# Kernel optimization log

Measured on AMD Instinct MI355X. Metric: run time of the kernel, lower is better.

The kernel has to match this reference:

```python
import jax, jax.numpy as jnp
import numpy as np

T, B, D, H = 32, 128, 256, 768
MAX_PONDER = 8
EPS = 0.01


def setup_inputs() -> dict:
    key = jax.random.key(0)
    ks = jax.random.split(key, 6)
    s = 1.0 / np.sqrt(H)
    return {
        "input_": jax.random.normal(ks[0], (T, B, D), jnp.float32),
        "W_ih": jax.random.uniform(ks[1], (H, D + 1), jnp.float32, -s, s),
        "W_hh": jax.random.uniform(ks[2], (H, H), jnp.float32, -s, s),
        "b_ih": jax.random.uniform(ks[3], (H,), jnp.float32, -s, s),
        "b_hh": jax.random.uniform(ks[4], (H,), jnp.float32, -s, s),
        "w_p": jax.random.uniform(ks[5], (H,), jnp.float32, -s, s),
        "b_p": jnp.ones((1,), jnp.float32),  # torch reset_parameters fills ponder bias with 1
    }


def reference(input_, W_ih, W_hh, b_ih, b_hh, w_p, b_p):
    T_, B_, D_ = input_.shape
    H_ = W_hh.shape[0]
    dt = input_.dtype
    hx0 = jnp.zeros((B_, H_), dt)

    def time_step(carry, x_t):
        hx, pcost = carry

        def ponder(c, _):
            hx_i, ah, ahx, sc, spc, mask, flag = c
            # input row with ponder flag (0 on first act step, 1 afterwards)
            x_in = jnp.concatenate([x_t, jnp.full((B_, 1), flag, dt)], axis=1)
            # ponder cost assigned for active rows before update
            spc = jnp.where(mask, -ah, spc)
            hx_new = jnp.tanh(x_in @ W_ih.T + b_ih + hx_i @ W_hh.T + b_hh)
            hx_i = jnp.where(mask[:, None], hx_new, hx_i)
            mf = mask.astype(dt)
            ahx = ahx + mf[:, None] * hx_new  # accum_hx += hx (as in source)
            h = jax.nn.sigmoid(hx_new @ w_p + b_p[0])
            ah2 = ah + mf * h
            p = h - jnp.maximum(ah2 - 1.0, 0.0)
            ahx = ahx + (mf * p)[:, None] * hx_new  # accum_hx += p*hx
            sc = sc + mf
            mask2 = ah2 < (1.0 - EPS)
            return (hx_i, ah2, ahx, sc, spc, mask2, jnp.ones((), dt)), None

        init = (hx,
                jnp.zeros((B_,), dt),           # accum_h
                jnp.zeros((B_, H_), dt),        # accum_hx
                jnp.zeros((B_,), dt),           # step_count
                jnp.zeros((B_,), dt),           # step_ponder_cost
                jnp.ones((B_,), bool),          # selector
                jnp.zeros((), dt))              # flag
        (hx_i, ah, ahx, sc, spc, mask, flag), _ = jax.lax.scan(
            ponder, init, None, length=MAX_PONDER)
        hx_out = ahx / sc[:, None]
        return (hx_out, pcost + spc), (hx_out, sc)

    (hx_last, pcost), (all_hx, steps) = jax.lax.scan(
        time_step, (hx0, jnp.zeros((B_,), dt)), input_)
    # all_hx: [T,B,H], hx: [1,B,H], ponder_cost: [B], ponder_times: [T,B]
    return all_hx, hx_last[None], pcost, steps
```

## Files before the change

### kernel.cpp

```cpp
#include <hip/hip_runtime.h>
#include <math.h>

#define TT 32
#define BB 128
#define DD 256
#define HH 768
#define MAXP 8

#define RG   8
#define RPG  16
#define CB   12
#define CS   64
#define NTH  256
#define NCH  24

#define OFF_LAST  ((size_t)TT * BB * HH)
#define OFF_PCOST (OFF_LAST + (size_t)BB * HH)
#define OFF_STEPS (OFF_PCOST + BB)

#define ASCOPE __HIP_MEMORY_SCOPE_AGENT

typedef __attribute__((ext_vector_type(8))) short s16x8;
typedef __attribute__((ext_vector_type(4))) float f32x4;
typedef unsigned long long ull;

static __device__ __forceinline__ unsigned short f2bf(float f) {
    unsigned u = __float_as_uint(f);
    u = (u + 0x7fffu + ((u >> 16) & 1u)) >> 16;
    return (unsigned short)u;
}
static __device__ __forceinline__ float bf2f(unsigned short h) {
    return __uint_as_float(((unsigned)h) << 16);
}

__launch_bounds__(NTH, 1)
__global__ void act_kernel(const float* __restrict__ x,
                           const float* __restrict__ Wih,
                           const float* __restrict__ Whh,
                           const float* __restrict__ bih,
                           const float* __restrict__ bhh,
                           const float* __restrict__ wpv,
                           const float* __restrict__ bp,
                           float* __restrict__ out,
                           unsigned* __restrict__ flags,
                           ull* __restrict__ hxe,
                           float* __restrict__ zpt)
{
    const int tid  = threadIdx.x;
    const int rg   = blockIdx.x & 7;
    const int cbk  = blockIdx.x >> 3;
    const int r0   = rg * RPG;
    const int c0   = cbk * CS;
    const int CT   = tid >> 6;
    const int lane = tid & 63;
    const int am   = lane & 15;
    const int aq   = lane >> 4;

    __shared__ s16x8 A_s[NCH * 64];
    __shared__ s16x8 WB_s[4 * 8 * 64];
    __shared__ s16x8 xA_s[8 * 64];
    __shared__ unsigned short hxn_s[RPG][72];
    __shared__ float zp4_s[RPG][4];
    __shared__ float zred_s[RPG][13];
    __shared__ float ah_s[RPG], spc_s[RPG], pc_s[RPG], w1p_s[RPG], sc_s[RPG], inv_s[RPG];
    __shared__ int   act_s[RPG];
    __shared__ int   nact_s;
    __shared__ float bias_s[CS], wflag_s[CS], wp_s[CS];
    __shared__ float bp_s;

    s16x8 Breg[NCH];
    {
        const float* wr = Whh + (size_t)(c0 + CT*16 + am) * HH + aq*8;
        for (int ch = 0; ch < NCH; ++ch) {
            float4 a0 = *(const float4*)(wr + ch*32);
            float4 a1 = *(const float4*)(wr + ch*32 + 4);
            union { s16x8 v; unsigned short e[8]; } u;
            u.e[0]=f2bf(a0.x); u.e[1]=f2bf(a0.y); u.e[2]=f2bf(a0.z); u.e[3]=f2bf(a0.w);
            u.e[4]=f2bf(a1.x); u.e[5]=f2bf(a1.y); u.e[6]=f2bf(a1.z); u.e[7]=f2bf(a1.w);
            Breg[ch] = u.v;
        }
    }
    for (int ch = 0; ch < 8; ++ch) {
        const float* wr = Wih + (size_t)(c0 + CT*16 + am) * (DD+1) + ch*32 + aq*8;
        union { s16x8 v; unsigned short e[8]; } u;
        #pragma unroll
        for (int j = 0; j < 8; ++j) u.e[j] = f2bf(wr[j]);
        WB_s[(CT*8 + ch)*64 + lane] = u.v;
    }
    if (tid < CS) {
        bias_s[tid]  = bih[c0+tid] + bhh[c0+tid];
        wflag_s[tid] = Wih[(size_t)(c0+tid)*(DD+1) + DD];
        wp_s[tid]    = wpv[c0+tid];
    }
    if (tid == 0) bp_s = bp[0];
    if (tid < RPG) pc_s[tid] = 0.f;
    {
        s16x8 z8 = {0,0,0,0,0,0,0,0};
        #pragma unroll
        for (int j = 0; j < 6; ++j) A_s[j*NTH + tid] = z8;
    }
    __syncthreads();

    float ahx[48];
    unsigned it = 0;

    for (int t = 0; t < TT; ++t) {
        #pragma unroll
        for (int j = 0; j < 2; ++j) {
            const int s = j*NTH + tid;
            const int ch = s >> 6;
            const float* xb = x + ((size_t)t*BB + r0 + am)*DD + ch*32 + aq*8;
            float4 a0 = *(const float4*)xb;
            float4 a1 = *(const float4*)(xb + 4);
            union { s16x8 v; unsigned short e[8]; } u;
            u.e[0]=f2bf(a0.x); u.e[1]=f2bf(a0.y); u.e[2]=f2bf(a0.z); u.e[3]=f2bf(a0.w);
            u.e[4]=f2bf(a1.x); u.e[5]=f2bf(a1.y); u.e[6]=f2bf(a1.z); u.e[7]=f2bf(a1.w);
            xA_s[s] = u.v;
        }
        if (tid < RPG) { ah_s[tid]=0.f; spc_s[tid]=0.f; sc_s[tid]=0.f; act_s[tid]=1; }
        #pragma unroll
        for (int qq = 0; qq < 48; ++qq) ahx[qq] = 0.f;
        __syncthreads();

        f32x4 xi;
        {
            f32x4 acc = {0.f,0.f,0.f,0.f};
            #pragma unroll
            for (int ch = 0; ch < 8; ++ch)
                acc = __builtin_amdgcn_mfma_f32_16x16x32_bf16(
                        xA_s[ch*64 + lane], WB_s[(CT*8 + ch)*64 + lane], acc, 0, 0, 0);
            const float bs = bias_s[CT*16 + am];
            xi[0]=acc[0]+bs; xi[1]=acc[1]+bs; xi[2]=acc[2]+bs; xi[3]=acc[3]+bs;
        }

        int pk = 0;
        for (;;) {
            const unsigned par = it & 1u;
            ull*   exch = hxe + (size_t)(rg*2 + par) * (NCH*64) * 2;
            float* zpb  = zpt + (size_t)(rg*2 + par) * (CB*16);

            f32x4 acc = xi;
            #pragma unroll
            for (int ch = 0; ch < NCH; ++ch)
                acc = __builtin_amdgcn_mfma_f32_16x16x32_bf16(
                        A_s[ch*64 + lane], Breg[ch], acc, 0, 0, 0);
            const float fl = pk ? wflag_s[CT*16 + am] : 0.f;
            #pragma unroll
            for (int r = 0; r < 4; ++r)
                hxn_s[aq*4 + r][CT*16 + am] = f2bf(tanhf(acc[r] + fl));
            __syncthreads();

            if (tid < 64) {
                const int r = tid >> 2, cq = tid & 3;
                float s = 0.f;
                #pragma unroll
                for (int i = 0; i < 16; ++i)
                    s += bf2f(hxn_s[r][cq*16 + i]) * wp_s[cq*16 + i];
                zp4_s[r][cq] = s;
            }
            __syncthreads();
            if (tid < RPG) {
                const float zp = zp4_s[tid][0] + zp4_s[tid][1] + zp4_s[tid][2] + zp4_s[tid][3];
                __hip_atomic_store(&zpb[cbk*16 + tid], zp, __ATOMIC_RELAXED, ASCOPE);
            }
            if (tid < 128) {
                const int chd = tid >> 6, l = tid & 63;
                const int pm = l & 15, pq = l >> 4;
                const int cbase = chd*32 + pq*8;
                const ull lo = *(const ull*)&hxn_s[pm][cbase];
                const ull hi = *(const ull*)&hxn_s[pm][cbase + 4];
                ull* dst = exch + (size_t)((2*cbk + chd)*64 + l)*2;
                __hip_atomic_store(dst,     lo, __ATOMIC_RELAXED, ASCOPE);
                __hip_atomic_store(dst + 1, hi, __ATOMIC_RELAXED, ASCOPE);
            }

            ++it;
            __syncthreads();
            if (tid < 64) {
                if (tid == 0)
                    __hip_atomic_store(&flags[rg*16 + cbk], it, __ATOMIC_RELAXED, ASCOPE);
                const int pi = tid % 12;
                unsigned v;
                do { v = __hip_atomic_load(&flags[rg*16 + pi], __ATOMIC_RELAXED, ASCOPE); }
                while (!__all((int)(v >= it)));
                __builtin_amdgcn_fence(__ATOMIC_ACQUIRE, "agent");
            }
            __syncthreads();

            ull nlo[6], nhi[6];
            #pragma unroll
            for (int j = 0; j < 6; ++j) {
                ull* src = exch + (size_t)(j*NTH + tid)*2;
                nlo[j] = __hip_atomic_load(src,     __ATOMIC_RELAXED, ASCOPE);
                nhi[j] = __hip_atomic_load(src + 1, __ATOMIC_RELAXED, ASCOPE);
            }
            if (tid < 192) {
                const int bb_ = tid >> 4, rr = tid & 15;
                zred_s[rr][bb_] = __hip_atomic_load(&zpb[bb_*16 + rr], __ATOMIC_RELAXED, ASCOPE);
            }
            __syncthreads();

            if (tid < RPG) {
                float w1p = 0.f;
                if (act_s[tid]) {
                    float z = 0.f;
                    #pragma unroll
                    for (int i2 = 0; i2 < CB; ++i2) z += zred_s[tid][i2];
                    const float h = 1.f / (1.f + expf(-(z + bp_s)));
                    spc_s[tid] = -ah_s[tid];
                    const float ah2 = ah_s[tid] + h;
                    const float p = h - fmaxf(ah2 - 1.f, 0.f);
                    w1p = 1.f + p;
                    sc_s[tid] += 1.f;
                    ah_s[tid] = ah2;
                    act_s[tid] = (ah2 < 0.99f) ? 1 : 0;
                }
                w1p_s[tid] = w1p;
            }
            __syncthreads();

            {
                const float w1 = w1p_s[am];
                const int   aa = act_s[am];
                #pragma unroll
                for (int j = 0; j < 6; ++j) {
                    const ull lo = nlo[j], hi = nhi[j];
                    #pragma unroll
                    for (int i = 0; i < 4; ++i) {
                        ahx[j*8 + i]     += w1 * bf2f((unsigned short)(lo >> (16*i)));
                        ahx[j*8 + 4 + i] += w1 * bf2f((unsigned short)(hi >> (16*i)));
                    }
                    if (aa) {
                        union { ull u[2]; s16x8 v; } cv; cv.u[0] = lo; cv.u[1] = hi;
                        A_s[j*NTH + tid] = cv.v;
                    }
                }
            }
            if (tid == 0) {
                int n = 0;
                #pragma unroll
                for (int r2 = 0; r2 < RPG; ++r2) n += act_s[r2];
                nact_s = n;
            }
            ++pk;
            __syncthreads();
            if (nact_s == 0 || pk == MAXP) break;
        }

        if (tid < RPG) {
            inv_s[tid] = 1.f / sc_s[tid];
            pc_s[tid] += spc_s[tid];
            if (cbk == 0) out[OFF_STEPS + (size_t)t*BB + r0 + tid] = sc_s[tid];
        }
        __syncthreads();
        {
            const float inv = inv_s[am];
            #pragma unroll
            for (int j = 0; j < 6; ++j) {
                const int ch = j*4 + CT;
                float o[8];
                #pragma unroll
                for (int i = 0; i < 8; ++i) o[i] = ahx[j*8 + i] * inv;
                union { s16x8 v; unsigned short e[8]; } u;
                #pragma unroll
                for (int i = 0; i < 8; ++i) u.e[i] = f2bf(o[i]);
                A_s[j*NTH + tid] = u.v;
                if (cbk == 0) {
                    float* op = out + ((size_t)t*BB + r0 + am)*HH + ch*32 + aq*8;
                    *(float4*)op       = make_float4(o[0], o[1], o[2], o[3]);
                    *(float4*)(op + 4) = make_float4(o[4], o[5], o[6], o[7]);
                    if (t == TT-1) {
                        float* lp = out + OFF_LAST + (size_t)(r0 + am)*HH + ch*32 + aq*8;
                        *(float4*)lp       = make_float4(o[0], o[1], o[2], o[3]);
                        *(float4*)(lp + 4) = make_float4(o[4], o[5], o[6], o[7]);
                    }
                }
            }
        }
        __syncthreads();
    }
    if (cbk == 0 && tid < RPG) out[OFF_PCOST + r0 + tid] = pc_s[tid];
}

extern "C" void kernel_launch(void* const* d_in, const int* in_sizes, int n_in,
                              void* d_out, int out_size, void* d_ws, size_t ws_size,
                              hipStream_t stream) {
    const float* x   = (const float*)d_in[0];
    const float* Wih = (const float*)d_in[1];
    const float* Whh = (const float*)d_in[2];
    const float* bih = (const float*)d_in[3];
    const float* bhh = (const float*)d_in[4];
    const float* wpv = (const float*)d_in[5];
    const float* bp  = (const float*)d_in[6];
    float* out = (float*)d_out;

    unsigned* flags = (unsigned*)d_ws;
    ull*      hxe   = (ull*)((char*)d_ws + 4096);
    float*    zpt   = (float*)((char*)d_ws + 4096 + (size_t)RG*2*NCH*64*16);

    hipMemsetAsync(d_ws, 0, 4096, stream);
    act_kernel<<<dim3(RG*CB), dim3(NTH), 0, stream>>>(
        x, Wih, Whh, bih, bhh, wpv, bp, out, flags, hxe, zpt);
}
```

Baseline: 395.0 us.

## Restructure ponder loop to cut block barriers and feed MFMA from exchange directly

Rewrites the inner ponder step so each warp loads the full exchanged hidden state straight from global memory into registers and feeds MFMA from there, instead of staging it through shared memory. Halting state is kept redundantly in per-lane registers, and each wave computes the active/done decision itself, which removes most of the block-wide syncthreads. A single wave now publishes hx and the ponder-logit partials, with a release fence before setting the flag. tanh is replaced by a fast exp-based formula and the first ponder step is peeled out. The costs are more global loads per wave and a cheaper tanh approximation that may lose some accuracy.

```diff
diff --git a/kernel.cpp b/kernel.cpp
--- a/kernel.cpp
+++ b/kernel.cpp
@@ -32,6 +32,11 @@
 static __device__ __forceinline__ float bf2f(unsigned short h) {
     return __uint_as_float(((unsigned)h) << 16);
 }
+static __device__ __forceinline__ float fast_tanh(float v) {
+    return 1.f - 2.f / (__expf(2.f * v) + 1.f);
+}
+
+union AU { float4 f; s16x8 s; unsigned short e[8]; };
 
 __launch_bounds__(NTH, 1)
 __global__ void act_kernel(const float* __restrict__ x,
@@ -43,7 +48,7 @@
                            const float* __restrict__ bp,
                            float* __restrict__ out,
                            unsigned* __restrict__ flags,
-                           ull* __restrict__ hxe,
+                           s16x8* __restrict__ hxe,
                            float* __restrict__ zpt)
 {
     const int tid  = threadIdx.x;
@@ -60,13 +65,7 @@
     __shared__ s16x8 WB_s[4 * 8 * 64];
     __shared__ s16x8 xA_s[8 * 64];
     __shared__ unsigned short hxn_s[RPG][72];
-    __shared__ float zp4_s[RPG][4];
-    __shared__ float zred_s[RPG][13];
-    __shared__ float ah_s[RPG], spc_s[RPG], pc_s[RPG], w1p_s[RPG], sc_s[RPG], inv_s[RPG];
-    __shared__ int   act_s[RPG];
-    __shared__ int   nact_s;
-    __shared__ float bias_s[CS], wflag_s[CS], wp_s[CS];
-    __shared__ float bp_s;
+    __shared__ float wp_s[CS];
 
     s16x8 Breg[NCH];
     {
@@ -87,22 +86,41 @@
         for (int j = 0; j < 8; ++j) u.e[j] = f2bf(wr[j]);
         WB_s[(CT*8 + ch)*64 + lane] = u.v;
     }
-    if (tid < CS) {
-        bias_s[tid]  = bih[c0+tid] + bhh[c0+tid];
-        wflag_s[tid] = Wih[(size_t)(c0+tid)*(DD+1) + DD];
-        wp_s[tid]    = wpv[c0+tid];
-    }
-    if (tid == 0) bp_s = bp[0];
-    if (tid < RPG) pc_s[tid] = 0.f;
+    if (tid < CS) wp_s[tid] = wpv[c0 + tid];
+    const int myc = c0 + CT*16 + am;
+    const float bs_lane = bih[myc] + bhh[myc];
+    const float wfl     = Wih[(size_t)myc*(DD+1) + DD];
+    const float bp0     = bp[0];
     {
         s16x8 z8 = {0,0,0,0,0,0,0,0};
         #pragma unroll
         for (int j = 0; j < 6; ++j) A_s[j*NTH + tid] = z8;
     }
-    __syncthreads();
-
-    float ahx[48];
+
+    float pc = 0.f;
     unsigned it = 0;
+
+    auto do_publish = [&]() {
+        const unsigned par = it & 1u;
+        s16x8* exw = hxe + (size_t)(rg*2 + par) * (NCH*64);
+        float* zpw = zpt + (size_t)(rg*2 + par) * (RPG*CB);
+        if (CT == 0) {
+            exw[(2*cbk)*64   + lane] = *(const s16x8*)&hxn_s[am][aq*8];
+            exw[(2*cbk+1)*64 + lane] = *(const s16x8*)&hxn_s[am][32 + aq*8];
+            const int zr = lane >> 2, zc = lane & 3;
+            float sz = 0.f;
+            #pragma unroll
+            for (int i = 0; i < 16; ++i)
+                sz += bf2f(hxn_s[zr][zc*16 + i]) * wp_s[zc*16 + i];
+            sz += __shfl_xor(sz, 1);
+            sz += __shfl_xor(sz, 2);
+            if (zc == 0) zpw[zr*CB + cbk] = sz;
+            __builtin_amdgcn_fence(__ATOMIC_RELEASE, "agent");
+            if (lane == 0)
+                __hip_atomic_store(&flags[rg*16 + cbk], it + 1u, __ATOMIC_RELAXED, ASCOPE);
+        }
+        ++it;
+    };
 
     for (int t = 0; t < TT; ++t) {
         #pragma unroll
@@ -117,169 +135,128 @@
             u.e[4]=f2bf(a1.x); u.e[5]=f2bf(a1.y); u.e[6]=f2bf(a1.z); u.e[7]=f2bf(a1.w);
             xA_s[s] = u.v;
         }
-        if (tid < RPG) { ah_s[tid]=0.f; spc_s[tid]=0.f; sc_s[tid]=0.f; act_s[tid]=1; }
-        #pragma unroll
-        for (int qq = 0; qq < 48; ++qq) ahx[qq] = 0.f;
         __syncthreads();
 
         f32x4 xi;
         {
-            f32x4 acc = {0.f,0.f,0.f,0.f};
+            f32x4 a = {0.f,0.f,0.f,0.f};
             #pragma unroll
             for (int ch = 0; ch < 8; ++ch)
-                acc = __builtin_amdgcn_mfma_f32_16x16x32_bf16(
-                        xA_s[ch*64 + lane], WB_s[(CT*8 + ch)*64 + lane], acc, 0, 0, 0);
-            const float bs = bias_s[CT*16 + am];
-            xi[0]=acc[0]+bs; xi[1]=acc[1]+bs; xi[2]=acc[2]+bs; xi[3]=acc[3]+bs;
-        }
-
-        int pk = 0;
-        for (;;) {
-            const unsigned par = it & 1u;
-            ull*   exch = hxe + (size_t)(rg*2 + par) * (NCH*64) * 2;
-            float* zpb  = zpt + (size_t)(rg*2 + par) * (CB*16);
-
+                a = __builtin_amdgcn_mfma_f32_16x16x32_bf16(
+                        xA_s[ch*64 + lane], WB_s[(CT*8 + ch)*64 + lane], a, 0, 0, 0);
+            xi[0]=a[0]+bs_lane; xi[1]=a[1]+bs_lane; xi[2]=a[2]+bs_lane; xi[3]=a[3]+bs_lane;
+        }
+
+        float ahx[48];
+        #pragma unroll
+        for (int q = 0; q < 48; ++q) ahx[q] = 0.f;
+        float ah = 0.f, sc = 0.f, spc = 0.f;
+        int act = 1;
+
+        {
             f32x4 acc = xi;
             #pragma unroll
             for (int ch = 0; ch < NCH; ++ch)
                 acc = __builtin_amdgcn_mfma_f32_16x16x32_bf16(
                         A_s[ch*64 + lane], Breg[ch], acc, 0, 0, 0);
-            const float fl = pk ? wflag_s[CT*16 + am] : 0.f;
             #pragma unroll
             for (int r = 0; r < 4; ++r)
-                hxn_s[aq*4 + r][CT*16 + am] = f2bf(tanhf(acc[r] + fl));
-            __syncthreads();
-
-            if (tid < 64) {
-                const int r = tid >> 2, cq = tid & 3;
-                float s = 0.f;
-                #pragma unroll
-                for (int i = 0; i < 16; ++i)
-                    s += bf2f(hxn_s[r][cq*16 + i]) * wp_s[cq*16 + i];
-                zp4_s[r][cq] = s;
-            }
-            __syncthreads();
-            if (tid < RPG) {
-                const float zp = zp4_s[tid][0] + zp4_s[tid][1] + zp4_s[tid][2] + zp4_s[tid][3];
-                __hip_atomic_store(&zpb[cbk*16 + tid], zp, __ATOMIC_RELAXED, ASCOPE);
-            }
-            if (tid < 128) {
-                const int chd = tid >> 6, l = tid & 63;
-                const int pm = l & 15, pq = l >> 4;
-                const int cbase = chd*32 + pq*8;
-                const ull lo = *(const ull*)&hxn_s[pm][cbase];
-                const ull hi = *(const ull*)&hxn_s[pm][cbase + 4];
-                ull* dst = exch + (size_t)((2*cbk + chd)*64 + l)*2;
-                __hip_atomic_store(dst,     lo, __ATOMIC_RELAXED, ASCOPE);
-                __hip_atomic_store(dst + 1, hi, __ATOMIC_RELAXED, ASCOPE);
-            }
-
-            ++it;
-            __syncthreads();
-            if (tid < 64) {
-                if (tid == 0)
-                    __hip_atomic_store(&flags[rg*16 + cbk], it, __ATOMIC_RELAXED, ASCOPE);
-                const int pi = tid % 12;
+                hxn_s[aq*4 + r][CT*16 + am] = f2bf(fast_tanh(acc[r]));
+        }
+        __syncthreads();
+        do_publish();
+
+        for (int pk = 1; ; ++pk) {
+            {
+                const int pi = lane % 12;
                 unsigned v;
                 do { v = __hip_atomic_load(&flags[rg*16 + pi], __ATOMIC_RELAXED, ASCOPE); }
                 while (!__all((int)(v >= it)));
-                __builtin_amdgcn_fence(__ATOMIC_ACQUIRE, "agent");
-            }
+            }
+            __builtin_amdgcn_fence(__ATOMIC_ACQUIRE, "agent");
+            const unsigned parR = (it - 1u) & 1u;
+            const s16x8* exr = hxe + (size_t)(rg*2 + parR) * (NCH*64);
+            const float* zpr = zpt + (size_t)(rg*2 + parR) * (RPG*CB);
+
+            const float4* zb4 = (const float4*)(zpr + am*CB);
+            const float4 z0 = zb4[0], z1 = zb4[1], z2 = zb4[2];
+            AU aload[NCH];
+            #pragma unroll
+            for (int ch = 0; ch < NCH; ++ch)
+                aload[ch].f = *(const float4*)&exr[ch*64 + lane];
+
+            const float z = ((z0.x+z0.y)+(z0.z+z0.w))
+                          + ((z1.x+z1.y)+(z1.z+z1.w))
+                          + ((z2.x+z2.y)+(z2.z+z2.w));
+            const float h = 1.f / (1.f + __expf(-(z + bp0)));
+            float w1 = 0.f;
+            if (act) {
+                spc = -ah;
+                ah += h;
+                w1 = 1.f + (h - fmaxf(ah - 1.f, 0.f));
+                sc += 1.f;
+                act = (ah < 0.99f) ? 1 : 0;
+            }
+            const bool done = __all(act == 0) || (pk == MAXP);
+
+            if (done) {
+                #pragma unroll
+                for (int ch = 0; ch < NCH; ++ch)
+                    if ((ch & 3) == CT) {
+                        const int j = ch >> 2;
+                        #pragma unroll
+                        for (int i = 0; i < 8; ++i)
+                            ahx[j*8 + i] += w1 * bf2f(aload[ch].e[i]);
+                    }
+                break;
+            }
+
+            f32x4 acc = xi;
+            #pragma unroll
+            for (int ch = 0; ch < NCH; ++ch)
+                acc = __builtin_amdgcn_mfma_f32_16x16x32_bf16(
+                        aload[ch].s, Breg[ch], acc, 0, 0, 0);
+            #pragma unroll
+            for (int ch = 0; ch < NCH; ++ch)
+                if ((ch & 3) == CT) {
+                    const int j = ch >> 2;
+                    #pragma unroll
+                    for (int i = 0; i < 8; ++i)
+                        ahx[j*8 + i] += w1 * bf2f(aload[ch].e[i]);
+                }
+            #pragma unroll
+            for (int r = 0; r < 4; ++r)
+                hxn_s[aq*4 + r][CT*16 + am] = f2bf(fast_tanh(acc[r] + wfl));
             __syncthreads();
-
-            ull nlo[6], nhi[6];
-            #pragma unroll
-            for (int j = 0; j < 6; ++j) {
-                ull* src = exch + (size_t)(j*NTH + tid)*2;
-                nlo[j] = __hip_atomic_load(src,     __ATOMIC_RELAXED, ASCOPE);
-                nhi[j] = __hip_atomic_load(src + 1, __ATOMIC_RELAXED, ASCOPE);
-            }
-            if (tid < 192) {
-                const int bb_ = tid >> 4, rr = tid & 15;
-                zred_s[rr][bb_] = __hip_atomic_load(&zpb[bb_*16 + rr], __ATOMIC_RELAXED, ASCOPE);
-            }
-            __syncthreads();
-
-            if (tid < RPG) {
-                float w1p = 0.f;
-                if (act_s[tid]) {
-                    float z = 0.f;
-                    #pragma unroll
-                    for (int i2 = 0; i2 < CB; ++i2) z += zred_s[tid][i2];
-                    const float h = 1.f / (1.f + expf(-(z + bp_s)));
-                    spc_s[tid] = -ah_s[tid];
-                    const float ah2 = ah_s[tid] + h;
-                    const float p = h - fmaxf(ah2 - 1.f, 0.f);
-                    w1p = 1.f + p;
-                    sc_s[tid] += 1.f;
-                    ah_s[tid] = ah2;
-                    act_s[tid] = (ah2 < 0.99f) ? 1 : 0;
+            do_publish();
+        }
+
+        const float inv = 1.f / sc;
+        pc += spc;
+        if (cbk == 0 && tid < RPG) out[OFF_STEPS + (size_t)t*BB + r0 + tid] = sc;
+        #pragma unroll
+        for (int j = 0; j < 6; ++j) {
+            const int ch = j*4 + CT;
+            float o[8];
+            #pragma unroll
+            for (int i = 0; i < 8; ++i) o[i] = ahx[j*8 + i] * inv;
+            union { s16x8 v; unsigned short e[8]; } u;
+            #pragma unroll
+            for (int i = 0; i < 8; ++i) u.e[i] = f2bf(o[i]);
+            A_s[ch*64 + lane] = u.v;
+            if (cbk == 0) {
+                float* op = out + ((size_t)t*BB + r0 + am)*HH + ch*32 + aq*8;
+                *(float4*)op       = make_float4(o[0], o[1], o[2], o[3]);
+                *(float4*)(op + 4) = make_float4(o[4], o[5], o[6], o[7]);
+                if (t == TT-1) {
+                    float* lp = out + OFF_LAST + (size_t)(r0 + am)*HH + ch*32 + aq*8;
+                    *(float4*)lp       = make_float4(o[0], o[1], o[2], o[3]);
+                    *(float4*)(lp + 4) = make_float4(o[4], o[5], o[6], o[7]);
                 }
-                w1p_s[tid] = w1p;
-            }
-            __syncthreads();
-
-            {
-                const float w1 = w1p_s[am];
-                const int   aa = act_s[am];
-                #pragma unroll
-                for (int j = 0; j < 6; ++j) {
-                    const ull lo = nlo[j], hi = nhi[j];
-                    #pragma unroll
-                    for (int i = 0; i < 4; ++i) {
-                        ahx[j*8 + i]     += w1 * bf2f((unsigned short)(lo >> (16*i)));
-                        ahx[j*8 + 4 + i] += w1 * bf2f((unsigned short)(hi >> (16*i)));
-                    }
-                    if (aa) {
-                        union { ull u[2]; s16x8 v; } cv; cv.u[0] = lo; cv.u[1] = hi;
-                        A_s[j*NTH + tid] = cv.v;
-                    }
-                }
-            }
-            if (tid == 0) {
-                int n = 0;
-                #pragma unroll
-                for (int r2 = 0; r2 < RPG; ++r2) n += act_s[r2];
-                nact_s = n;
-            }
-            ++pk;
-            __syncthreads();
-            if (nact_s == 0 || pk == MAXP) break;
-        }
-
-        if (tid < RPG) {
-            inv_s[tid] = 1.f / sc_s[tid];
-            pc_s[tid] += spc_s[tid];
-            if (cbk == 0) out[OFF_STEPS + (size_t)t*BB + r0 + tid] = sc_s[tid];
-        }
-        __syncthreads();
-        {
-            const float inv = inv_s[am];
-            #pragma unroll
-            for (int j = 0; j < 6; ++j) {
-                const int ch = j*4 + CT;
-                float o[8];
-                #pragma unroll
-                for (int i = 0; i < 8; ++i) o[i] = ahx[j*8 + i] * inv;
-                union { s16x8 v; unsigned short e[8]; } u;
-                #pragma unroll
-                for (int i = 0; i < 8; ++i) u.e[i] = f2bf(o[i]);
-                A_s[j*NTH + tid] = u.v;
-                if (cbk == 0) {
-                    float* op = out + ((size_t)t*BB + r0 + am)*HH + ch*32 + aq*8;
-                    *(float4*)op       = make_float4(o[0], o[1], o[2], o[3]);
-                    *(float4*)(op + 4) = make_float4(o[4], o[5], o[6], o[7]);
-                    if (t == TT-1) {
-                        float* lp = out + OFF_LAST + (size_t)(r0 + am)*HH + ch*32 + aq*8;
-                        *(float4*)lp       = make_float4(o[0], o[1], o[2], o[3]);
-                        *(float4*)(lp + 4) = make_float4(o[4], o[5], o[6], o[7]);
-                    }
-                }
-            }
-        }
-        __syncthreads();
-    }
-    if (cbk == 0 && tid < RPG) out[OFF_PCOST + r0 + tid] = pc_s[tid];
+            }
+        }
+    }
+    if (cbk == 0 && tid < RPG) out[OFF_PCOST + r0 + tid] = pc;
 }
 
 extern "C" void kernel_launch(void* const* d_in, const int* in_sizes, int n_in,
@@ -295,7 +272,7 @@
     float* out = (float*)d_out;
 
     unsigned* flags = (unsigned*)d_ws;
-    ull*      hxe   = (ull*)((char*)d_ws + 4096);
+    s16x8*    hxe   = (s16x8*)((char*)d_ws + 4096);
     float*    zpt   = (float*)((char*)d_ws + 4096 + (size_t)RG*2*NCH*64*16);
 
     hipMemsetAsync(d_ws, 0, 4096, stream);
```

Result: slower. 624.6 us (+58.1%).
